# Kernel optimization log

Measured on AMD Instinct MI355X. Metric: run time of the kernel, lower is better.

Reference implementation:

```python
import jax, jax.numpy as jnp
import numpy as np

N_HEADS = 16
HEAD_DIM = 64
DIM = 1024
BATCH = 2
SEQ = 2048


def setup_inputs() -> dict:
    key = jax.random.key(0)
    ks = jax.random.split(key, 6)
    hd = N_HEADS * HEAD_DIM
    scale_in = 1.0 / np.sqrt(DIM)
    scale_out = 1.0 / np.sqrt(hd)
    return {
        "x": jax.random.normal(ks[0], (BATCH, SEQ, DIM), dtype=jnp.float32),
        "Wq": jax.random.normal(ks[1], (DIM, hd), dtype=jnp.float32) * scale_in,
        "Wk": jax.random.normal(ks[2], (DIM, hd), dtype=jnp.float32) * scale_in,
        "Wv": jax.random.normal(ks[3], (DIM, hd), dtype=jnp.float32) * scale_in,
        "Wo": jax.random.normal(ks[4], (hd, DIM), dtype=jnp.float32) * scale_out,
        "bo": jnp.zeros((DIM,), dtype=jnp.float32),
    }


def reference(x, Wq, Wk, Wv, Wo, bo):
    b, s, _ = x.shape
    # QKV projections (bias-free Dense), reshape to [b, s, h, d]
    q = (x @ Wq).reshape(b, s, N_HEADS, HEAD_DIM)
    k = (x @ Wk).reshape(b, s, N_HEADS, HEAD_DIM)
    v = (x @ Wv).reshape(b, s, N_HEADS, HEAD_DIM)
    # scores [b, h, i, k], softmax over last axis (keys)
    dot = jnp.einsum('bihd,bkhd->bhik', q, k)
    w = jax.nn.softmax(dot / jnp.sqrt(jnp.float32(HEAD_DIM)), axis=-1)
    # weighted sum of values -> [b, i, h, d]
    a = jnp.einsum('bhij,bjhd->bihd', w, v)
    a = a.reshape(b, s, N_HEADS * HEAD_DIM)
    return a @ Wo + bo
```

## Files before the change

kernel.cpp:

```cpp
#include <hip/hip_runtime.h>
#include <hip/hip_bf16.h>
#include <math.h>

#define NH     16
#define HDIM   64
#define SEQ    2048
#define BATCH  2
#define MTOT   (BATCH*SEQ)
#define DMODEL 1024
#define HD3    3072
#define QKW    2048

#define QSCALE 0.18033688011112043f

typedef __attribute__((ext_vector_type(8))) short  short8;
typedef __attribute__((ext_vector_type(8))) ushort ushort8;
typedef __attribute__((ext_vector_type(4))) ushort ushortx4;
typedef __attribute__((ext_vector_type(4))) float  f32x4;
typedef __attribute__((ext_vector_type(2))) unsigned int u32x2;

__device__ __forceinline__ ushort f2b(float f) {
    __hip_bfloat16 h = __float2bfloat16(f);
    return *reinterpret_cast<ushort*>(&h);
}
__device__ __forceinline__ uint cvtpk(float a, float b) {
    uint r;
    asm("v_cvt_pk_bf16_f32 %0, %1, %2" : "=v"(r) : "v"(a), "v"(b));
    return r;
}
__device__ __forceinline__ float fexp2(float x) {
    float r;
    asm("v_exp_f32 %0, %1" : "=v"(r) : "v"(x));
    return r;
}

__device__ __forceinline__ void gload_lds16(const void* g, void* l) {
    __builtin_amdgcn_global_load_lds(
        (const __attribute__((address_space(1))) unsigned int*)g,
        (__attribute__((address_space(3))) unsigned int*)l, 16, 0, 0);
}

__global__ __launch_bounds__(256) void prep_kernel(
    const float* __restrict__ x,
    const float* __restrict__ Wq, const float* __restrict__ Wk,
    const float* __restrict__ Wv, const float* __restrict__ Wo,
    ushort* __restrict__ xb, ushort* __restrict__ Wt, ushort* __restrict__ Wot)
{
    __shared__ float s[64][33];
    const int tid = threadIdx.x;
    const int bid = blockIdx.x;

    if (bid < 2048) {
        const int i = bid * 256 + tid;
        const float4* p = (const float4*)(x + (size_t)i * 8);
        const float4 v0 = p[0], v1 = p[1];
        ushort8 o;
        o[0] = f2b(v0.x); o[1] = f2b(v0.y); o[2] = f2b(v0.z); o[3] = f2b(v0.w);
        o[4] = f2b(v1.x); o[5] = f2b(v1.y); o[6] = f2b(v1.z); o[7] = f2b(v1.w);
        *(ushort8*)(xb + (size_t)i * 8) = o;
        return;
    }

    const int t   = bid - 2048;
    const int z   = t >> 9;
    const int rem = t & 511;
    const int n0  = (rem & 15) * 64;
    const int k0  = (rem >> 4) * 32;
    const float* W = (z == 0) ? Wq : (z == 1) ? Wk : (z == 2) ? Wv : Wo;
    ushort* D = (z == 3) ? Wot : Wt + (size_t)z * DMODEL * DMODEL;

    #pragma unroll
    for (int i = 0; i < 8; ++i) {
        const int idx = tid + i * 256;
        const int n = idx & 63, k = idx >> 6;
        s[n][k] = W[(size_t)(k0 + k) * DMODEL + n0 + n];
    }
    __syncthreads();
    const int n  = tid >> 2;
    const int kc = (tid & 3) * 8;
    ushort8 o;
    #pragma unroll
    for (int j = 0; j < 8; ++j) o[j] = f2b(s[n][kc + j]);
    *(ushort8*)(&D[(size_t)(n0 + n) * DMODEL + k0 + kc]) = o;
}

template <typename OT, int BN>
__global__ __launch_bounds__(256) void gemm_mfma_kernel(
    const ushort* __restrict__ A, const ushort* __restrict__ Bt,
    const float* __restrict__ bias, OT* __restrict__ C,
    ushort* __restrict__ Vt,
    int M, int N, int K, int ldc, int qcols, float qscale, int nx)
{
    constexpr int NI = BN / 32;
    __shared__ __align__(16) ushort As[2][128 * 32];
    __shared__ __align__(16) ushort Bs[2][BN * 32];

    const int tid  = threadIdx.x;
    const int lane = tid & 63;
    const int lr   = lane & 15;
    const int lg   = lane >> 4;
    const int w    = tid >> 6;
    const int wm   = w >> 1, wn = w & 1;

    const int d   = blockIdx.x;
    const int xcd = d & 7;
    const int i   = d >> 3;
    const int m0 = (xcd * 4 + i / nx) * 128;
    const int n0 = (i % nx) * BN;

    f32x4 acc[4][NI];
    #pragma unroll
    for (int mi = 0; mi < 4; ++mi)
        #pragma unroll
        for (int ni = 0; ni < NI; ++ni) acc[mi][ni] = f32x4{0.f, 0.f, 0.f, 0.f};

    #pragma unroll
    for (int i2 = 0; i2 < 2; ++i2) {
        const int ch  = i2 * 256 + tid;
        const int row = ch >> 2, ccd = ch & 3, ccs = ccd ^ ((row >> 1) & 3);
        gload_lds16(&A[(size_t)(m0 + row) * K + ccs * 8], &As[0][ch * 8]);
    }
    #pragma unroll
    for (int i2 = 0; i2 < BN / 64; ++i2) {
        const int ch  = i2 * 256 + tid;
        const int row = ch >> 2, ccd = ch & 3, ccs = ccd ^ ((row >> 1) & 3);
        gload_lds16(&Bt[(size_t)(n0 + row) * K + ccs * 8], &Bs[0][ch * 8]);
    }

    for (int kt = 0; kt < K; kt += 32) {
        const int cur = (kt >> 5) & 1;
        __syncthreads();

        if (kt + 32 < K) {
            #pragma unroll
            for (int i2 = 0; i2 < 2; ++i2) {
                const int ch  = i2 * 256 + tid;
                const int row = ch >> 2, ccd = ch & 3, ccs = ccd ^ ((row >> 1) & 3);
                gload_lds16(&A[(size_t)(m0 + row) * K + kt + 32 + ccs * 8],
                            &As[cur ^ 1][ch * 8]);
            }
            #pragma unroll
            for (int i2 = 0; i2 < BN / 64; ++i2) {
                const int ch  = i2 * 256 + tid;
                const int row = ch >> 2, ccd = ch & 3, ccs = ccd ^ ((row >> 1) & 3);
                gload_lds16(&Bt[(size_t)(n0 + row) * K + kt + 32 + ccs * 8],
                            &Bs[cur ^ 1][ch * 8]);
            }
        }

        short8 af[4], bf[NI];
        #pragma unroll
        for (int mi = 0; mi < 4; ++mi) {
            const int row = wm * 64 + mi * 16 + lr;
            af[mi] = *(const short8*)(&As[cur][row * 32 + (lg ^ ((row >> 1) & 3)) * 8]);
        }
        #pragma unroll
        for (int ni = 0; ni < NI; ++ni) {
            const int row = wn * (BN / 2) + ni * 16 + lr;
            bf[ni] = *(const short8*)(&Bs[cur][row * 32 + (lg ^ ((row >> 1) & 3)) * 8]);
        }
        #pragma unroll
        for (int mi = 0; mi < 4; ++mi)
            #pragma unroll
            for (int ni = 0; ni < NI; ++ni)
                acc[mi][ni] = __builtin_amdgcn_mfma_f32_16x16x32_bf16(
                    af[mi], bf[ni], acc[mi][ni], 0, 0, 0);
    }

    if (Vt != nullptr && n0 >= 2048) {
        #pragma unroll
        for (int mi = 0; mi < 4; ++mi) {
            const int mb = m0 + wm * 64 + mi * 16 + lg * 4;
            const int bb = mb >> 11, ss = mb & 2047;
            #pragma unroll
            for (int ni = 0; ni < NI; ++ni) {
                const int n  = n0 + wn * (BN / 2) + ni * 16 + lr - 2048;
                const int h  = n >> 6, dd = n & 63;
                ushortx4 o;
                #pragma unroll
                for (int r = 0; r < 4; ++r) o[r] = f2b(acc[mi][ni][r]);
                *(ushortx4*)(&Vt[(((size_t)bb * NH + h) * HDIM + dd) * SEQ + ss]) = o;
            }
        }
        return;
    }

    #pragma unroll
    for (int mi = 0; mi < 4; ++mi) {
        #pragma unroll
        for (int ni = 0; ni < NI; ++ni) {
            const int n = n0 + wn * (BN / 2) + ni * 16 + lr;
            const float bv = bias ? bias[n] : 0.f;
            const float sc = (n < qcols) ? qscale : 1.f;
            #pragma unroll
            for (int r = 0; r < 4; ++r) {
                const int m = m0 + wm * 64 + mi * 16 + lg * 4 + r;
                const float v = (acc[mi][ni][r] + bv) * sc;
                if constexpr (sizeof(OT) == 2)
                    C[(size_t)m * ldc + n] = f2b(v);
                else
                    C[(size_t)m * ldc + n] = v;
            }
        }
    }
}

__global__ __launch_bounds__(256) void flash_attn_kernel(
    const ushort* __restrict__ QK, const ushort* __restrict__ Vt,
    ushort* __restrict__ Aout)
{
    __shared__ __align__(16) char LDS[2][16384];

    const int tid  = threadIdx.x;
    const int lane = tid & 63;
    const int w    = tid >> 6;
    const int lr   = lane & 15;
    const int lg   = lane >> 4;

    const int dblk = blockIdx.x;
    const int xcd  = dblk & 7;
    const int i    = dblk >> 3;
    const int bh   = xcd * 4 + (i >> 4);
    const int qt   = i & 15;
    const int b    = bh >> 4;
    const int h    = bh & 15;
    const int q0   = qt * 128;

    const size_t qb0 = ((size_t)(b * SEQ + q0 + w * 32 + 0 * 16 + lr)) * QKW + h * HDIM;
    const size_t qb1 = ((size_t)(b * SEQ + q0 + w * 32 + 1 * 16 + lr)) * QKW + h * HDIM;
    short8 qf0[2], qf1[2];
    qf0[0] = *(const short8*)(&QK[qb0 + lg * 8]);
    qf0[1] = *(const short8*)(&QK[qb0 + 32 + lg * 8]);
    qf1[0] = *(const short8*)(&QK[qb1 + lg * 8]);
    qf1[1] = *(const short8*)(&QK[qb1 + 32 + lg * 8]);

    f32x4 O0[4], O1[4];
    #pragma unroll
    for (int dn = 0; dn < 4; ++dn) { O0[dn] = f32x4{0,0,0,0}; O1[dn] = f32x4{0,0,0,0}; }
    float li0 = 0.f, li1 = 0.f;

    const size_t kbase  = (size_t)b * SEQ * QKW + 1024 + h * HDIM;
    const size_t vtbase = ((size_t)(b * NH + h)) * HDIM * SEQ;

    const int r0   = tid >> 3;
    const int s0   = (tid & 7) ^ (r0 & 7);
    const size_t off0 = (size_t)r0 * QKW + s0 * 8;
    const size_t off1 = off0 + (size_t)32 * QKW;

    {
        const ushort* Kg = QK + kbase;
        const ushort* Vg = Vt + vtbase;
        gload_lds16(Kg + off0, &LDS[0][tid * 16]);
        gload_lds16(Kg + off1, &LDS[0][4096 + tid * 16]);
        gload_lds16(Vg + off0, &LDS[0][8192 + tid * 16]);
        gload_lds16(Vg + off1, &LDS[0][12288 + tid * 16]);
    }

    int fbase[2];
    #pragma unroll
    for (int s = 0; s < 2; ++s)
        fbase[s] = lr * 128 + (((s * 4 + lg) * 16) ^ ((lr & 7) << 4));
    int vfb[2][2];
    #pragma unroll
    for (int s = 0; s < 2; ++s)
        #pragma unroll
        for (int hh = 0; hh < 2; ++hh)
            vfb[s][hh] = lr * 128 + ((64 * s + 32 * hh + 8 * lg) ^ ((lr & 7) << 4));

    for (int kt = 0; kt < SEQ; kt += 64) {
        const int cur = (kt >> 6) & 1;
        __syncthreads();

        if (kt + 64 < SEQ) {
            const ushort* Kg = QK + kbase + (size_t)(kt + 64) * QKW;
            const ushort* Vg = Vt + vtbase + (kt + 64);
            char* Lb = &LDS[cur ^ 1][0];
            gload_lds16(Kg + off0, Lb + tid * 16);
            gload_lds16(Kg + off1, Lb + 4096 + tid * 16);
            gload_lds16(Vg + off0, Lb + 8192 + tid * 16);
            gload_lds16(Vg + off1, Lb + 12288 + tid * 16);
        }

        const char* Kb = &LDS[cur][0]    + fbase[0];
        const char* Kc = &LDS[cur][0]    + fbase[1];
        const char* Vb = &LDS[cur][8192];

        float p0[4][4], p1[4][4];
        __builtin_amdgcn_s_setprio(1);
        #pragma unroll
        for (int sub = 0; sub < 4; ++sub) {
            f32x4 a0 = {0,0,0,0}, a1 = {0,0,0,0};
            short8 kf0 = *(const short8*)(Kb + sub * 2048);
            short8 kf1 = *(const short8*)(Kc + sub * 2048);
            a0 = __builtin_amdgcn_mfma_f32_16x16x32_bf16(kf0, qf0[0], a0, 0, 0, 0);
            a0 = __builtin_amdgcn_mfma_f32_16x16x32_bf16(kf1, qf0[1], a0, 0, 0, 0);
            a1 = __builtin_amdgcn_mfma_f32_16x16x32_bf16(kf0, qf1[0], a1, 0, 0, 0);
            a1 = __builtin_amdgcn_mfma_f32_16x16x32_bf16(kf1, qf1[1], a1, 0, 0, 0);
            #pragma unroll
            for (int r = 0; r < 4; ++r) { p0[sub][r] = a0[r]; p1[sub][r] = a1[r]; }
        }
        __builtin_amdgcn_s_setprio(0);

        #pragma unroll
        for (int sub = 0; sub < 4; ++sub)
            #pragma unroll
            for (int r = 0; r < 4; ++r) {
                p0[sub][r] = fexp2(p0[sub][r]);
                p1[sub][r] = fexp2(p1[sub][r]);
            }
        {
            const float a0 = (p0[0][0] + p0[0][1]) + (p0[0][2] + p0[0][3]);
            const float a1 = (p0[1][0] + p0[1][1]) + (p0[1][2] + p0[1][3]);
            const float a2 = (p0[2][0] + p0[2][1]) + (p0[2][2] + p0[2][3]);
            const float a3 = (p0[3][0] + p0[3][1]) + (p0[3][2] + p0[3][3]);
            li0 += (a0 + a1) + (a2 + a3);
            const float b0 = (p1[0][0] + p1[0][1]) + (p1[0][2] + p1[0][3]);
            const float b1 = (p1[1][0] + p1[1][1]) + (p1[1][2] + p1[1][3]);
            const float b2 = (p1[2][0] + p1[2][1]) + (p1[2][2] + p1[2][3]);
            const float b3 = (p1[3][0] + p1[3][1]) + (p1[3][2] + p1[3][3]);
            li1 += (b0 + b1) + (b2 + b3);
        }

        short8 pf0[2], pf1[2];
        #pragma unroll
        for (int s = 0; s < 2; ++s) {
            union { short8 v; uint u[4]; } u0, u1;
            u0.u[0] = cvtpk(p0[2*s+0][0], p0[2*s+0][1]);
            u0.u[1] = cvtpk(p0[2*s+0][2], p0[2*s+0][3]);
            u0.u[2] = cvtpk(p0[2*s+1][0], p0[2*s+1][1]);
            u0.u[3] = cvtpk(p0[2*s+1][2], p0[2*s+1][3]);
            pf0[s] = u0.v;
            u1.u[0] = cvtpk(p1[2*s+0][0], p1[2*s+0][1]);
            u1.u[1] = cvtpk(p1[2*s+0][2], p1[2*s+0][3]);
            u1.u[2] = cvtpk(p1[2*s+1][0], p1[2*s+1][1]);
            u1.u[3] = cvtpk(p1[2*s+1][2], p1[2*s+1][3]);
            pf1[s] = u1.v;
        }

        __builtin_amdgcn_s_setprio(1);
        #pragma unroll
        for (int dn = 0; dn < 4; ++dn) {
            #pragma unroll
            for (int s = 0; s < 2; ++s) {
                union { short8 v; u32x2 u2[2]; } vu;
                vu.u2[0] = *(const u32x2*)(Vb + dn * 2048 + vfb[s][0]);
                vu.u2[1] = *(const u32x2*)(Vb + dn * 2048 + vfb[s][1]);
                O0[dn] = __builtin_amdgcn_mfma_f32_16x16x32_bf16(vu.v, pf0[s], O0[dn], 0, 0, 0);
                O1[dn] = __builtin_amdgcn_mfma_f32_16x16x32_bf16(vu.v, pf1[s], O1[dn], 0, 0, 0);
            }
        }
        __builtin_amdgcn_s_setprio(0);
    }

    {
        float lt = li0;
        lt += __shfl_xor(lt, 16);
        lt += __shfl_xor(lt, 32);
        const float inv = 1.f / lt;
        const size_t obase =
            ((size_t)(b * SEQ + q0 + w * 32 + 0 * 16 + lr)) * DMODEL + h * HDIM;
        #pragma unroll
        for (int dn = 0; dn < 4; ++dn) {
            ushortx4 o;
            #pragma unroll
            for (int r = 0; r < 4; ++r) o[r] = f2b(O0[dn][r] * inv);
            *(ushortx4*)(&Aout[obase + dn * 16 + lg * 4]) = o;
        }
    }
    {
        float lt = li1;
        lt += __shfl_xor(lt, 16);
        lt += __shfl_xor(lt, 32);
        const float inv = 1.f / lt;
        const size_t obase =
            ((size_t)(b * SEQ + q0 + w * 32 + 1 * 16 + lr)) * DMODEL + h * HDIM;
        #pragma unroll
        for (int dn = 0; dn < 4; ++dn) {
            ushortx4 o;
            #pragma unroll
            for (int r = 0; r < 4; ++r) o[r] = f2b(O1[dn][r] * inv);
            *(ushortx4*)(&Aout[obase + dn * 16 + lg * 4]) = o;
        }
    }
}

extern "C" void kernel_launch(void* const* d_in, const int* in_sizes, int n_in,
                              void* d_out, int out_size, void* d_ws, size_t ws_size,
                              hipStream_t stream)
{
    const float* x  = (const float*)d_in[0];
    const float* Wq = (const float*)d_in[1];
    const float* Wk = (const float*)d_in[2];
    const float* Wv = (const float*)d_in[3];
    const float* Wo = (const float*)d_in[4];
    const float* bo = (const float*)d_in[5];
    float* out = (float*)d_out;

    ushort* xb  = (ushort*)d_ws;
    ushort* Wt  = xb  + (size_t)MTOT * DMODEL;
    ushort* Wot = Wt  + (size_t)HD3  * DMODEL;
    ushort* QK  = Wot + (size_t)DMODEL * DMODEL;
    ushort* Vt  = QK  + (size_t)MTOT * QKW;
    ushort* Ab  = xb;

    dim3 blk(256);

    prep_kernel<<<dim3(4096), blk, 0, stream>>>(x, Wq, Wk, Wv, Wo, xb, Wt, Wot);

    gemm_mfma_kernel<ushort, 128><<<dim3(768), blk, 0, stream>>>(
        xb, Wt, nullptr, QK, Vt, MTOT, HD3, DMODEL, QKW, DMODEL, QSCALE, 24);

    flash_attn_kernel<<<dim3(512), blk, 0, stream>>>(QK, Vt, Ab);

    gemm_mfma_kernel<float, 64><<<dim3(512), blk, 0, stream>>>(
        Ab, Wot, bo, out, nullptr, MTOT, DMODEL, DMODEL, DMODEL, 0, 1.f, 16);
}
```

Baseline: 117.8 us.

## Split attention key tiles across wave pairs with LDS reduction of partial outputs

The flash attention kernel now launches 512 threads per block. Each pair of waves shares the same 32 query rows, and each wave in the pair handles half of every 64-key tile. Each thread issues half as many global-to-LDS loads, and the two waves' partial O accumulators and row sums are combined through LDS at the end. The aim is more waves in flight to hide latency and more parallelism per block. In exchange it adds a final LDS reduction and extra barriers, and halves the MFMA work per wave per tile, which may raise barrier overhead relative to compute.

```diff
diff --git a/kernel.cpp b/kernel.cpp
--- a/kernel.cpp
+++ b/kernel.cpp
@@ -205,15 +205,18 @@
     }
 }
 
-__global__ __launch_bounds__(256) void flash_attn_kernel(
+__global__ __launch_bounds__(512, 4) void flash_attn_kernel(
     const ushort* __restrict__ QK, const ushort* __restrict__ Vt,
     ushort* __restrict__ Aout)
 {
     __shared__ __align__(16) char LDS[2][16384];
+    __shared__ float li_x[8][16];
 
     const int tid  = threadIdx.x;
     const int lane = tid & 63;
     const int w    = tid >> 6;
+    const int qw   = w >> 1;
+    const int kw   = w & 1;
     const int lr   = lane & 15;
     const int lg   = lane >> 4;
 
@@ -226,8 +229,8 @@
     const int h    = bh & 15;
     const int q0   = qt * 128;
 
-    const size_t qb0 = ((size_t)(b * SEQ + q0 + w * 32 + 0 * 16 + lr)) * QKW + h * HDIM;
-    const size_t qb1 = ((size_t)(b * SEQ + q0 + w * 32 + 1 * 16 + lr)) * QKW + h * HDIM;
+    const size_t qb0 = ((size_t)(b * SEQ + q0 + qw * 32 + 0 * 16 + lr)) * QKW + h * HDIM;
+    const size_t qb1 = ((size_t)(b * SEQ + q0 + qw * 32 + 1 * 16 + lr)) * QKW + h * HDIM;
     short8 qf0[2], qf1[2];
     qf0[0] = *(const short8*)(&QK[qb0 + lg * 8]);
     qf0[1] = *(const short8*)(&QK[qb0 + 32 + lg * 8]);
@@ -242,56 +245,44 @@
     const size_t kbase  = (size_t)b * SEQ * QKW + 1024 + h * HDIM;
     const size_t vtbase = ((size_t)(b * NH + h)) * HDIM * SEQ;
 
-    const int r0   = tid >> 3;
-    const int s0   = (tid & 7) ^ (r0 & 7);
-    const size_t off0 = (size_t)r0 * QKW + s0 * 8;
-    const size_t off1 = off0 + (size_t)32 * QKW;
+    const int r0 = tid >> 3;
+    const int s0 = (tid & 7) ^ (r0 & 7);
+    const size_t offK = (size_t)r0 * QKW + s0 * 8;
 
     {
-        const ushort* Kg = QK + kbase;
-        const ushort* Vg = Vt + vtbase;
-        gload_lds16(Kg + off0, &LDS[0][tid * 16]);
-        gload_lds16(Kg + off1, &LDS[0][4096 + tid * 16]);
-        gload_lds16(Vg + off0, &LDS[0][8192 + tid * 16]);
-        gload_lds16(Vg + off1, &LDS[0][12288 + tid * 16]);
+        gload_lds16(QK + kbase + offK, &LDS[0][tid * 16]);
+        gload_lds16(Vt + vtbase + offK, &LDS[0][8192 + tid * 16]);
     }
 
     int fbase[2];
     #pragma unroll
     for (int s = 0; s < 2; ++s)
-        fbase[s] = lr * 128 + (((s * 4 + lg) * 16) ^ ((lr & 7) << 4));
-    int vfb[2][2];
-    #pragma unroll
-    for (int s = 0; s < 2; ++s)
-        #pragma unroll
-        for (int hh = 0; hh < 2; ++hh)
-            vfb[s][hh] = lr * 128 + ((64 * s + 32 * hh + 8 * lg) ^ ((lr & 7) << 4));
+        fbase[s] = kw * 4096 + lr * 128 + (((s * 4 + lg) * 16) ^ ((lr & 7) << 4));
+    int vfb[2];
+    #pragma unroll
+    for (int hh = 0; hh < 2; ++hh)
+        vfb[hh] = lr * 128 + ((kw * 64 + 32 * hh + 8 * lg) ^ ((lr & 7) << 4));
 
     for (int kt = 0; kt < SEQ; kt += 64) {
         const int cur = (kt >> 6) & 1;
         __syncthreads();
 
         if (kt + 64 < SEQ) {
-            const ushort* Kg = QK + kbase + (size_t)(kt + 64) * QKW;
-            const ushort* Vg = Vt + vtbase + (kt + 64);
             char* Lb = &LDS[cur ^ 1][0];
-            gload_lds16(Kg + off0, Lb + tid * 16);
-            gload_lds16(Kg + off1, Lb + 4096 + tid * 16);
-            gload_lds16(Vg + off0, Lb + 8192 + tid * 16);
-            gload_lds16(Vg + off1, Lb + 12288 + tid * 16);
-        }
-
-        const char* Kb = &LDS[cur][0]    + fbase[0];
-        const char* Kc = &LDS[cur][0]    + fbase[1];
+            gload_lds16(QK + kbase + (size_t)(kt + 64) * QKW + offK, Lb + tid * 16);
+            gload_lds16(Vt + vtbase + (kt + 64) + offK, Lb + 8192 + tid * 16);
+        }
+
+        const char* Kb = &LDS[cur][0];
         const char* Vb = &LDS[cur][8192];
 
-        float p0[4][4], p1[4][4];
+        float p0[2][4], p1[2][4];
         __builtin_amdgcn_s_setprio(1);
         #pragma unroll
-        for (int sub = 0; sub < 4; ++sub) {
+        for (int sub = 0; sub < 2; ++sub) {
             f32x4 a0 = {0,0,0,0}, a1 = {0,0,0,0};
-            short8 kf0 = *(const short8*)(Kb + sub * 2048);
-            short8 kf1 = *(const short8*)(Kc + sub * 2048);
+            short8 kf0 = *(const short8*)(Kb + sub * 2048 + fbase[0]);
+            short8 kf1 = *(const short8*)(Kb + sub * 2048 + fbase[1]);
             a0 = __builtin_amdgcn_mfma_f32_16x16x32_bf16(kf0, qf0[0], a0, 0, 0, 0);
             a0 = __builtin_amdgcn_mfma_f32_16x16x32_bf16(kf1, qf0[1], a0, 0, 0, 0);
             a1 = __builtin_amdgcn_mfma_f32_16x16x32_bf16(kf0, qf1[0], a1, 0, 0, 0);
@@ -302,84 +293,80 @@
         __builtin_amdgcn_s_setprio(0);
 
         #pragma unroll
-        for (int sub = 0; sub < 4; ++sub)
+        for (int sub = 0; sub < 2; ++sub)
             #pragma unroll
             for (int r = 0; r < 4; ++r) {
                 p0[sub][r] = fexp2(p0[sub][r]);
                 p1[sub][r] = fexp2(p1[sub][r]);
             }
+        li0 += ((p0[0][0] + p0[0][1]) + (p0[0][2] + p0[0][3]))
+             + ((p0[1][0] + p0[1][1]) + (p0[1][2] + p0[1][3]));
+        li1 += ((p1[0][0] + p1[0][1]) + (p1[0][2] + p1[0][3]))
+             + ((p1[1][0] + p1[1][1]) + (p1[1][2] + p1[1][3]));
+
+        short8 pf0, pf1;
         {
-            const float a0 = (p0[0][0] + p0[0][1]) + (p0[0][2] + p0[0][3]);
-            const float a1 = (p0[1][0] + p0[1][1]) + (p0[1][2] + p0[1][3]);
-            const float a2 = (p0[2][0] + p0[2][1]) + (p0[2][2] + p0[2][3]);
-            const float a3 = (p0[3][0] + p0[3][1]) + (p0[3][2] + p0[3][3]);
-            li0 += (a0 + a1) + (a2 + a3);
-            const float b0 = (p1[0][0] + p1[0][1]) + (p1[0][2] + p1[0][3]);
-            const float b1 = (p1[1][0] + p1[1][1]) + (p1[1][2] + p1[1][3]);
-            const float b2 = (p1[2][0] + p1[2][1]) + (p1[2][2] + p1[2][3]);
-            const float b3 = (p1[3][0] + p1[3][1]) + (p1[3][2] + p1[3][3]);
-            li1 += (b0 + b1) + (b2 + b3);
-        }
-
-        short8 pf0[2], pf1[2];
-        #pragma unroll
-        for (int s = 0; s < 2; ++s) {
             union { short8 v; uint u[4]; } u0, u1;
-            u0.u[0] = cvtpk(p0[2*s+0][0], p0[2*s+0][1]);
-            u0.u[1] = cvtpk(p0[2*s+0][2], p0[2*s+0][3]);
-            u0.u[2] = cvtpk(p0[2*s+1][0], p0[2*s+1][1]);
-            u0.u[3] = cvtpk(p0[2*s+1][2], p0[2*s+1][3]);
-            pf0[s] = u0.v;
-            u1.u[0] = cvtpk(p1[2*s+0][0], p1[2*s+0][1]);
-            u1.u[1] = cvtpk(p1[2*s+0][2], p1[2*s+0][3]);
-            u1.u[2] = cvtpk(p1[2*s+1][0], p1[2*s+1][1]);
-            u1.u[3] = cvtpk(p1[2*s+1][2], p1[2*s+1][3]);
-            pf1[s] = u1.v;
+            u0.u[0] = cvtpk(p0[0][0], p0[0][1]);
+            u0.u[1] = cvtpk(p0[0][2], p0[0][3]);
+            u0.u[2] = cvtpk(p0[1][0], p0[1][1]);
+            u0.u[3] = cvtpk(p0[1][2], p0[1][3]);
+            pf0 = u0.v;
+            u1.u[0] = cvtpk(p1[0][0], p1[0][1]);
+            u1.u[1] = cvtpk(p1[0][2], p1[0][3]);
+            u1.u[2] = cvtpk(p1[1][0], p1[1][1]);
+            u1.u[3] = cvtpk(p1[1][2], p1[1][3]);
+            pf1 = u1.v;
         }
 
         __builtin_amdgcn_s_setprio(1);
         #pragma unroll
         for (int dn = 0; dn < 4; ++dn) {
-            #pragma unroll
-            for (int s = 0; s < 2; ++s) {
-                union { short8 v; u32x2 u2[2]; } vu;
-                vu.u2[0] = *(const u32x2*)(Vb + dn * 2048 + vfb[s][0]);
-                vu.u2[1] = *(const u32x2*)(Vb + dn * 2048 + vfb[s][1]);
-                O0[dn] = __builtin_amdgcn_mfma_f32_16x16x32_bf16(vu.v, pf0[s], O0[dn], 0, 0, 0);
-                O1[dn] = __builtin_amdgcn_mfma_f32_16x16x32_bf16(vu.v, pf1[s], O1[dn], 0, 0, 0);
-            }
+            union { short8 v; u32x2 u2[2]; } vu;
+            vu.u2[0] = *(const u32x2*)(Vb + dn * 2048 + vfb[0]);
+            vu.u2[1] = *(const u32x2*)(Vb + dn * 2048 + vfb[1]);
+            O0[dn] = __builtin_amdgcn_mfma_f32_16x16x32_bf16(vu.v, pf0, O0[dn], 0, 0, 0);
+            O1[dn] = __builtin_amdgcn_mfma_f32_16x16x32_bf16(vu.v, pf1, O1[dn], 0, 0, 0);
         }
         __builtin_amdgcn_s_setprio(0);
     }
 
-    {
-        float lt = li0;
-        lt += __shfl_xor(lt, 16);
-        lt += __shfl_xor(lt, 32);
-        const float inv = 1.f / lt;
-        const size_t obase =
-            ((size_t)(b * SEQ + q0 + w * 32 + 0 * 16 + lr)) * DMODEL + h * HDIM;
+    li0 += __shfl_xor(li0, 16); li0 += __shfl_xor(li0, 32);
+    li1 += __shfl_xor(li1, 16); li1 += __shfl_xor(li1, 32);
+
+    __syncthreads();
+    char* Xf = &LDS[0][0];
+    if (kw == 1) {
         #pragma unroll
         for (int dn = 0; dn < 4; ++dn) {
-            ushortx4 o;
-            #pragma unroll
-            for (int r = 0; r < 4; ++r) o[r] = f2b(O0[dn][r] * inv);
-            *(ushortx4*)(&Aout[obase + dn * 16 + lg * 4]) = o;
-        }
-    }
-    {
-        float lt = li1;
-        lt += __shfl_xor(lt, 16);
-        lt += __shfl_xor(lt, 32);
-        const float inv = 1.f / lt;
-        const size_t obase =
-            ((size_t)(b * SEQ + q0 + w * 32 + 1 * 16 + lr)) * DMODEL + h * HDIM;
+            *(f32x4*)(Xf + ((qw * 2 + 0) * 4 + dn) * 1024 + lane * 16) = O0[dn];
+            *(f32x4*)(Xf + ((qw * 2 + 1) * 4 + dn) * 1024 + lane * 16) = O1[dn];
+        }
+        if (lane < 16) {
+            li_x[qw * 2 + 0][lane] = li0;
+            li_x[qw * 2 + 1][lane] = li1;
+        }
+    }
+    __syncthreads();
+    if (kw == 0) {
+        const float inv0 = 1.f / (li0 + li_x[qw * 2 + 0][lr]);
+        const float inv1 = 1.f / (li1 + li_x[qw * 2 + 1][lr]);
+        const size_t ob0 =
+            ((size_t)(b * SEQ + q0 + qw * 32 + 0 * 16 + lr)) * DMODEL + h * HDIM;
+        const size_t ob1 =
+            ((size_t)(b * SEQ + q0 + qw * 32 + 1 * 16 + lr)) * DMODEL + h * HDIM;
         #pragma unroll
         for (int dn = 0; dn < 4; ++dn) {
-            ushortx4 o;
-            #pragma unroll
-            for (int r = 0; r < 4; ++r) o[r] = f2b(O1[dn][r] * inv);
-            *(ushortx4*)(&Aout[obase + dn * 16 + lg * 4]) = o;
+            const f32x4 a0 = *(const f32x4*)(Xf + ((qw * 2 + 0) * 4 + dn) * 1024 + lane * 16);
+            const f32x4 a1 = *(const f32x4*)(Xf + ((qw * 2 + 1) * 4 + dn) * 1024 + lane * 16);
+            ushortx4 o0, o1;
+            #pragma unroll
+            for (int r = 0; r < 4; ++r) {
+                o0[r] = f2b((O0[dn][r] + a0[r]) * inv0);
+                o1[r] = f2b((O1[dn][r] + a1[r]) * inv1);
+            }
+            *(ushortx4*)(&Aout[ob0 + dn * 16 + lg * 4]) = o0;
+            *(ushortx4*)(&Aout[ob1 + dn * 16 + lg * 4]) = o1;
         }
     }
 }
@@ -410,7 +397,7 @@
     gemm_mfma_kernel<ushort, 128><<<dim3(768), blk, 0, stream>>>(
         xb, Wt, nullptr, QK, Vt, MTOT, HD3, DMODEL, QKW, DMODEL, QSCALE, 24);
 
-    flash_attn_kernel<<<dim3(512), blk, 0, stream>>>(QK, Vt, Ab);
+    flash_attn_kernel<<<dim3(512), dim3(512), 0, stream>>>(QK, Vt, Ab);
 
     gemm_mfma_kernel<float, 64><<<dim3(512), blk, 0, stream>>>(
         Ab, Wot, bo, out, nullptr, MTOT, DMODEL, DMODEL, DMODEL, 0, 1.f, 16);
```

After: 114.7 us (median of 2 runs). 1.03x faster.
